# Optimization experiments

Hardware: AMD Instinct MI355X
Metric: run time of the kernel (lower is better)

## Reference

```python
import jax, jax.numpy as jnp
import numpy as np

B = 64          # number of graphs
N_PER = 512     # nodes per graph (equal counts required by final view)
D = 64          # hidden_channels
R = 4           # channel-attention reduction


def setup_inputs() -> dict:
    key = jax.random.key(0)
    k1, k2, k3, k4, k5 = jax.random.split(key, 5)
    M = B * N_PER
    x = jax.random.normal(k1, (M, D), dtype=jnp.float32)
    batch = jnp.repeat(jnp.arange(B, dtype=jnp.int32), N_PER)  # sorted, equal segments
    # channel_attention mode=1 params (torch Linear: y = x @ W.T + b)
    s1 = 1.0 / np.sqrt(D)
    s2 = 1.0 / np.sqrt(D // R)
    W1 = jax.random.uniform(k2, (D // R, D), jnp.float32, -s1, s1)
    b1 = jax.random.uniform(k3, (D // R,), jnp.float32, -s1, s1)
    W2 = jax.random.uniform(k4, (D, D // R), jnp.float32, -s2, s2)
    b2 = jax.random.uniform(k5, (D,), jnp.float32, -s2, s2)
    return {"x": x, "batch": batch, "W1": W1, "b1": b1, "W2": W2, "b2": b2}


def reference(x, batch, W1, b1, W2, b2):
    M, d = x.shape
    # ---- channel_attention (mode=1, sigmoid gate) ----
    sums = jax.ops.segment_sum(x, batch, num_segments=B)                 # [B, D]
    cnts = jax.ops.segment_sum(jnp.ones((M, 1), x.dtype), batch, num_segments=B)
    gap = sums / cnts                                                    # scatter_mean
    h = jax.nn.leaky_relu(gap @ W1.T + b1, negative_slope=0.01)
    imp = jax.nn.sigmoid(h @ W2.T + b2)                                  # [B, D]
    xg = x * imp[batch]                                                  # repeat_interleave broadcast
    # ---- per-node outer product + triu vectorization ----
    # einsum('ik,kj->kij', x.T, x)[k] = outer(x[k], x[k]); take upper triangle (incl diag)
    iu0, iu1 = jnp.triu_indices(d)                                       # row-major triu order
    triu = xg[:, iu0] * xg[:, iu1]                                       # [M, D(D+1)/2]
    return triu.reshape(B, -1)
```

## Files before the change

kernel.cpp:

```cpp
#include <hip/hip_runtime.h>
#include <math.h>

#define NB_GRAPHS 64
#define NPER 512
#define DCH 64
#define DR 16
#define TRIU4 520

typedef float vfloat4 __attribute__((ext_vector_type(4)));


__global__ __launch_bounds__(512) void gap_mlp_kernel(
    const float* __restrict__ x,
    const float* __restrict__ W1, const float* __restrict__ b1,
    const float* __restrict__ W2, const float* __restrict__ b2,
    float* __restrict__ imp,
    unsigned int* __restrict__ tbl)
{
    __shared__ float part[32][64];
    __shared__ float sgap[64];
    __shared__ float sh[16];

    const int b   = blockIdx.x;
    const int tid = threadIdx.x;
    const int c4  = tid & 15;
    const int rg  = tid >> 4;

    const float4* xb = reinterpret_cast<const float4*>(x + (size_t)b * NPER * DCH);
    float4 acc = {0.f, 0.f, 0.f, 0.f};
    #pragma unroll
    for (int k = 0; k < 16; ++k) {
        float4 t = xb[(size_t)(rg + 32 * k) * 16 + c4];
        acc.x += t.x; acc.y += t.y; acc.z += t.z; acc.w += t.w;
    }
    part[rg][c4 * 4 + 0] = acc.x;
    part[rg][c4 * 4 + 1] = acc.y;
    part[rg][c4 * 4 + 2] = acc.z;
    part[rg][c4 * 4 + 3] = acc.w;
    __syncthreads();

    if (tid < 64) {
        float t = 0.f;
        #pragma unroll
        for (int g = 0; g < 32; ++g) t += part[g][tid];
        sgap[tid] = t * (1.0f / 512.0f);
    }
    __syncthreads();

    if (tid < DR) {
        float a = b1[tid];
        #pragma unroll
        for (int k = 0; k < 64; ++k) a += sgap[k] * W1[tid * 64 + k];
        sh[tid] = a >= 0.f ? a : 0.01f * a;
    }
    __syncthreads();

    if (tid < 64) {
        float a = b2[tid];
        #pragma unroll
        for (int j = 0; j < DR; ++j) a += sh[j] * W2[tid * DR + j];
        imp[b * 64 + tid] = 1.0f / (1.0f + expf(-a));
    }

    if (b == 0) {
        for (int t4 = tid; t4 < TRIU4; t4 += 512) {
            unsigned int pi = 0, pj = 0;
            #pragma unroll
            for (int e = 0; e < 4; ++e) {
                int tt = t4 * 4 + e;
                int ii = 0, rem = tt;
                while (rem >= 64 - ii) { rem -= 64 - ii; ++ii; }
                int jj = ii + rem;
                unsigned int ai = ((((unsigned)ii & 3u) << 4) | ((unsigned)ii >> 2)) << 2;
                unsigned int aj = ((((unsigned)jj & 3u) << 4) | ((unsigned)jj >> 2)) << 2;
                pi |= ai << (8 * e);
                pj |= aj << (8 * e);
            }
            tbl[t4]         = pi;
            tbl[TRIU4 + t4] = pj;
        }
    }
}

__global__ __launch_bounds__(256) void sop_kernel(
    const float* __restrict__ x,
    const float* __restrict__ imp,
    const unsigned int* __restrict__ tbl,
    float* __restrict__ out)
{
    __shared__ float v[4][4][64];

    const int tid  = threadIdx.x;
    const int w    = tid >> 6;
    const int lane = tid & 63;
    const int m0   = blockIdx.x * 16;
    const int b    = m0 >> 9;

    unsigned int ti[9], tj[9];
    #pragma unroll
    for (int k = 0; k < 9; ++k) {
        const int t4 = k * 64 + lane;
        const int t4c = (t4 < TRIU4) ? t4 : 0;
        ti[k] = tbl[t4c];
        tj[k] = tbl[TRIU4 + t4c];
    }

    const float4 xv  = reinterpret_cast<const float4*>(x + (size_t)(m0 + 4 * w) * DCH)[lane];
    const float4 iv4 = reinterpret_cast<const float4*>(imp + ((size_t)b << 6))[lane & 15];
    {
        const int n  = lane >> 4;
        const int cc = lane & 15;
        float* vn = &v[w][n][0];
        vn[0 * 16 + cc] = xv.x * iv4.x;
        vn[1 * 16 + cc] = xv.y * iv4.y;
        vn[2 * 16 + cc] = xv.z * iv4.z;
        vn[3 * 16 + cc] = xv.w * iv4.w;
    }

    #pragma unroll
    for (int it = 0; it < 4; ++it) {
        const int m = m0 + 4 * w + it;
        const char* vb = reinterpret_cast<const char*>(&v[w][it][0]);
        vfloat4* ob = reinterpret_cast<vfloat4*>(out) + (size_t)m * TRIU4;
        #pragma unroll
        for (int k = 0; k < 9; ++k) {
            if (k < 8 || lane < 8) {
                const unsigned int pi = ti[k], pj = tj[k];
                vfloat4 o;
                o.x = *reinterpret_cast<const float*>(vb + (pi & 255u))
                    * *reinterpret_cast<const float*>(vb + (pj & 255u));
                o.y = *reinterpret_cast<const float*>(vb + ((pi >> 8) & 255u))
                    * *reinterpret_cast<const float*>(vb + ((pj >> 8) & 255u));
                o.z = *reinterpret_cast<const float*>(vb + ((pi >> 16) & 255u))
                    * *reinterpret_cast<const float*>(vb + ((pj >> 16) & 255u));
                o.w = *reinterpret_cast<const float*>(vb + (pi >> 24))
                    * *reinterpret_cast<const float*>(vb + (pj >> 24));
                __builtin_nontemporal_store(o, &ob[k * 64 + lane]);
            }
        }
    }
}

extern "C" void kernel_launch(void* const* d_in, const int* in_sizes, int n_in,
                              void* d_out, int out_size, void* d_ws, size_t ws_size,
                              hipStream_t stream) {
    const float* x  = (const float*)d_in[0];
    const float* W1 = (const float*)d_in[2];
    const float* b1 = (const float*)d_in[3];
    const float* W2 = (const float*)d_in[4];
    const float* b2 = (const float*)d_in[5];
    float* out = (float*)d_out;
    float* imp = (float*)d_ws;
    unsigned int* tbl = reinterpret_cast<unsigned int*>((float*)d_ws + 4096);

    gap_mlp_kernel<<<NB_GRAPHS, 512, 0, stream>>>(x, W1, b1, W2, b2, imp, tbl);
    sop_kernel<<<(NB_GRAPHS * NPER) / 16, 256, 0, stream>>>(x, imp, tbl, out);
}
```

Before: 296.9 us.

## Use persistent 256-block grid for outer-product kernel with batched regular stores

```diff
diff --git a/kernel.cpp b/kernel.cpp
--- a/kernel.cpp
+++ b/kernel.cpp
@@ -6,8 +6,6 @@
 #define DCH 64
 #define DR 16
 #define TRIU4 520
-
-typedef float vfloat4 __attribute__((ext_vector_type(4)));
 
 
 __global__ __launch_bounds__(512) void gap_mlp_kernel(
@@ -82,60 +80,67 @@
     }
 }
 
-__global__ __launch_bounds__(256) void sop_kernel(
+__global__ __launch_bounds__(512, 2) void sop_kernel(
     const float* __restrict__ x,
     const float* __restrict__ imp,
     const unsigned int* __restrict__ tbl,
     float* __restrict__ out)
 {
-    __shared__ float v[4][4][64];
+    __shared__ float v[8][4][64];
 
     const int tid  = threadIdx.x;
     const int w    = tid >> 6;
     const int lane = tid & 63;
-    const int m0   = blockIdx.x * 16;
-    const int b    = m0 >> 9;
+    const int n    = lane >> 4;
+    const int cc   = lane & 15;
 
     unsigned int ti[9], tj[9];
     #pragma unroll
     for (int k = 0; k < 9; ++k) {
-        const int t4 = k * 64 + lane;
+        const int t4  = k * 64 + lane;
         const int t4c = (t4 < TRIU4) ? t4 : 0;
         ti[k] = tbl[t4c];
         tj[k] = tbl[TRIU4 + t4c];
     }
 
-    const float4 xv  = reinterpret_cast<const float4*>(x + (size_t)(m0 + 4 * w) * DCH)[lane];
-    const float4 iv4 = reinterpret_cast<const float4*>(imp + ((size_t)b << 6))[lane & 15];
-    {
-        const int n  = lane >> 4;
-        const int cc = lane & 15;
-        float* vn = &v[w][n][0];
-        vn[0 * 16 + cc] = xv.x * iv4.x;
-        vn[1 * 16 + cc] = xv.y * iv4.y;
-        vn[2 * 16 + cc] = xv.z * iv4.z;
-        vn[3 * 16 + cc] = xv.w * iv4.w;
-    }
+    for (int r = 0; r < 4; ++r) {
+        const int chunk = r * 256 + (int)blockIdx.x;
+        const int m0    = chunk * 32;
+        const int b     = m0 >> 9;
+        const int mw    = m0 + 4 * w;
 
-    #pragma unroll
-    for (int it = 0; it < 4; ++it) {
-        const int m = m0 + 4 * w + it;
-        const char* vb = reinterpret_cast<const char*>(&v[w][it][0]);
-        vfloat4* ob = reinterpret_cast<vfloat4*>(out) + (size_t)m * TRIU4;
+        const float4 xv  = reinterpret_cast<const float4*>(x + (size_t)mw * DCH)[lane];
+        const float4 iv4 = reinterpret_cast<const float4*>(imp + ((size_t)b << 6))[cc];
+        {
+            float* vn = &v[w][n][0];
+            vn[0 * 16 + cc] = xv.x * iv4.x;
+            vn[1 * 16 + cc] = xv.y * iv4.y;
+            vn[2 * 16 + cc] = xv.z * iv4.z;
+            vn[3 * 16 + cc] = xv.w * iv4.w;
+        }
+
         #pragma unroll
-        for (int k = 0; k < 9; ++k) {
-            if (k < 8 || lane < 8) {
+        for (int it = 0; it < 4; ++it) {
+            const char* vb = reinterpret_cast<const char*>(&v[w][it][0]);
+            float4 o[9];
+            #pragma unroll
+            for (int k = 0; k < 9; ++k) {
                 const unsigned int pi = ti[k], pj = tj[k];
-                vfloat4 o;
-                o.x = *reinterpret_cast<const float*>(vb + (pi & 255u))
-                    * *reinterpret_cast<const float*>(vb + (pj & 255u));
-                o.y = *reinterpret_cast<const float*>(vb + ((pi >> 8) & 255u))
-                    * *reinterpret_cast<const float*>(vb + ((pj >> 8) & 255u));
-                o.z = *reinterpret_cast<const float*>(vb + ((pi >> 16) & 255u))
-                    * *reinterpret_cast<const float*>(vb + ((pj >> 16) & 255u));
-                o.w = *reinterpret_cast<const float*>(vb + (pi >> 24))
-                    * *reinterpret_cast<const float*>(vb + (pj >> 24));
-                __builtin_nontemporal_store(o, &ob[k * 64 + lane]);
+                o[k].x = *reinterpret_cast<const float*>(vb + (pi & 255u))
+                       * *reinterpret_cast<const float*>(vb + (pj & 255u));
+                o[k].y = *reinterpret_cast<const float*>(vb + ((pi >> 8) & 255u))
+                       * *reinterpret_cast<const float*>(vb + ((pj >> 8) & 255u));
+                o[k].z = *reinterpret_cast<const float*>(vb + ((pi >> 16) & 255u))
+                       * *reinterpret_cast<const float*>(vb + ((pj >> 16) & 255u));
+                o[k].w = *reinterpret_cast<const float*>(vb + (pi >> 24))
+                       * *reinterpret_cast<const float*>(vb + (pj >> 24));
+            }
+            float4* ob = reinterpret_cast<float4*>(out) + (size_t)(mw + it) * TRIU4;
+            #pragma unroll
+            for (int k = 0; k < 9; ++k) {
+                if (k < 8 || lane < 8) {
+                    ob[k * 64 + lane] = o[k];
+                }
             }
         }
     }
@@ -154,5 +159,5 @@
     unsigned int* tbl = reinterpret_cast<unsigned int*>((float*)d_ws + 4096);
 
     gap_mlp_kernel<<<NB_GRAPHS, 512, 0, stream>>>(x, W1, b1, W2, b2, imp, tbl);
-    sop_kernel<<<(NB_GRAPHS * NPER) / 16, 256, 0, stream>>>(x, imp, tbl, out);
+    sop_kernel<<<256, 512, 0, stream>>>(x, imp, tbl, out);
 }
```

Result: no change. 299.8 us (+1.0%).
